# Kernel optimization log

Hardware: AMD Instinct MI355X
Metric: run time of the kernel (lower is better)

The kernel has to match this reference:

```python
import jax, jax.numpy as jnp
import numpy as np
import math

B, L, D, H = 2, 4096, 1024, 16
DH = D // H


def _build_table(seq_len):
    # Faithful port of build_hierarchical_index_lookup_table (static, host-side).
    assert seq_len & (seq_len - 1) == 0
    levels = int(math.log2(seq_len))
    max_valid = 2 * seq_len - 3
    idx = np.full((seq_len, levels), -1, dtype=np.int64)
    cm = np.zeros((seq_len, levels), dtype=bool)
    for n in range(seq_len):
        c = n
        for lvl in range(levels):
            if lvl == 0:
                nxt = c ^ 1
                pair = c
            else:
                nxt = (c // 2 + seq_len) ^ 1
                pair = c // 2 + seq_len
            if nxt > max_valid:
                break
            if pair < nxt:
                cm[n, lvl] = True
            idx[n, lvl] = nxt
            c = nxt
    return idx, cm


def setup_inputs() -> dict:
    rng = jax.random.key(0)
    ks = jax.random.split(rng, 8)
    s = 0.02  # init scale for weights
    idx, cm = _build_table(L)
    return {
        "query": jax.random.normal(ks[0], (B, L, D), jnp.float32),
        "key": jax.random.normal(ks[1], (B, L, D), jnp.float32),
        "value": jax.random.normal(ks[2], (B, L, D), jnp.float32),
        "Wq": jax.random.normal(ks[3], (D, D), jnp.float32) * s,
        "Wk": jax.random.normal(ks[4], (D, D), jnp.float32) * s,
        "Wv": jax.random.normal(ks[5], (D, D), jnp.float32) * s,
        "Wo": jax.random.normal(ks[6], (D, D), jnp.float32) * s,
        "bo": jax.random.normal(ks[7], (D,), jnp.float32) * s,
        "idx_table": jnp.asarray(idx),        # [L, log2(L)] int64
        "causal_mask": jnp.asarray(cm),       # [L, log2(L)] bool
    }


def reference(query, key, value, Wq, Wk, Wv, Wo, bo, idx_table, causal_mask):
    Bq, Lq, Dm = query.shape
    scale = 1.0 / math.sqrt(DH)

    def heads(x, W):  # nn.Linear (no bias) + split heads -> [B,H,L,Dh]
        return (x @ W.T).reshape(Bq, Lq, H, DH).transpose(0, 2, 1, 3)

    Q = heads(query, Wq)
    K = heads(key, Wk)
    V = heads(value, Wv)

    # Build binary-tree hierarchy. Pair weights come from softmax of ZERO
    # logits (Q_parent starts as zeros in the source), so w0 = w1 = 0.5 exactly.
    Ks, Vs = [K], [V]
    while Ks[-1].shape[2] > 1:
        k, v = Ks[-1], Vs[-1]
        Lc = k.shape[2]
        k2 = k.reshape(Bq, H, Lc // 2, 2, DH)
        v2 = v.reshape(Bq, H, Lc // 2, 2, DH)
        Ks.append(0.5 * (k2[:, :, :, 0] + k2[:, :, :, 1]))
        Vs.append(v2[:, :, :, 0] + v2[:, :, :, 1])
    flatK = jnp.concatenate(Ks, axis=2)  # [B,H,2L-1,Dh]
    flatV = jnp.concatenate(Vs, axis=2)

    # Gather neighbor nodes across levels: [B,H,L,levels,Dh]
    nk = flatK[:, :, idx_table]
    nv = flatV[:, :, idx_table]

    self_logits = jnp.einsum('bhnd,bhnd->bhn', Q, K) * scale
    nbr_logits = jnp.einsum('bhld,bhlnd->bhln', Q, nk) * scale
    nbr_logits = jnp.where(causal_mask[None, None], -jnp.inf, nbr_logits)

    all_logits = jnp.concatenate([self_logits[..., None], nbr_logits], axis=-1)
    w = jax.nn.softmax(all_logits, axis=-1)           # [B,H,L,1+levels]
    all_v = jnp.concatenate([V[:, :, :, None, :], nv], axis=3)
    out = jnp.einsum('bhln,bhlnd->bhld', w, all_v)    # [B,H,L,Dh]
    out = out.transpose(0, 2, 1, 3).reshape(Bq, Lq, Dm)
    return out @ Wo.T + bo
```

## Files before the change

### kernel.cpp

```cpp
#include <hip/hip_runtime.h>
#include <cstdint>
#include <cstddef>


typedef __bf16 bf16;
typedef __bf16 bf16x8 __attribute__((ext_vector_type(8)));
typedef __bf16 bf16x4 __attribute__((ext_vector_type(4)));
typedef float  f32x4  __attribute__((ext_vector_type(4)));

#define L_SEQ  4096
#define NFLAT  8192

__device__ __forceinline__ int off_l(int l) { return 8192 - (8192 >> l); }

__device__ __forceinline__ void glds16(const bf16* g, bf16* l) {
  __builtin_amdgcn_global_load_lds(
      (const __attribute__((address_space(1))) unsigned int*)g,
      (__attribute__((address_space(3))) unsigned int*)l, 16, 0, 0);
}

#define MEMFENCE asm volatile("" ::: "memory")
__device__ __forceinline__ void barrier_raw() {
  MEMFENCE; __builtin_amdgcn_s_barrier(); MEMFENCE;
}

__device__ __forceinline__ int swz(int b) { return b ^ (((b >> 9) & 1) << 5); }
__device__ __forceinline__ int la(int row, int col) {
  return ((((row >> 4) << 1) + (col >> 5)) << 10) + ((row & 15) << 6) + ((col & 31) << 1);
}

__global__ __launch_bounds__(256) void cvtall_kernel(
    const float* __restrict__ q, const float* __restrict__ k, const float* __restrict__ v,
    const float* __restrict__ wq, const float* __restrict__ wk,
    const float* __restrict__ wv, const float* __restrict__ wo,
    bf16* __restrict__ qx, bf16* __restrict__ kx, bf16* __restrict__ vx,
    bf16* __restrict__ wqx, bf16* __restrict__ wkx, bf16* __restrict__ wvx,
    bf16* __restrict__ wox) {
  for (int i = blockIdx.x * 256 + threadIdx.x; i < 3670016; i += 524288) {
    int g = i;
    const float* s; bf16* d;
    if (g < 3145728) {
      const int t = g >> 20; g &= 1048575;
      s = (t == 0) ? q : (t == 1) ? k : v;
      d = (t == 0) ? qx : (t == 1) ? kx : vx;
    } else {
      int gg = g - 3145728;
      const int t = gg >> 17; g = gg & 131071;
      s = (t == 0) ? wq : (t == 1) ? wk : (t == 2) ? wv : wo;
      d = (t == 0) ? wqx : (t == 1) ? wkx : (t == 2) ? wvx : wox;
    }
    const float4 v0 = ((const float4*)s)[(size_t)g * 2];
    const float4 v1 = ((const float4*)s)[(size_t)g * 2 + 1];
    bf16x8 o;
    o[0] = (bf16)v0.x; o[1] = (bf16)v0.y; o[2] = (bf16)v0.z; o[3] = (bf16)v0.w;
    o[4] = (bf16)v1.x; o[5] = (bf16)v1.y; o[6] = (bf16)v1.z; o[7] = (bf16)v1.w;
    *(bf16x8*)(d + (size_t)g * 8) = o;
  }
}

#define BUFB 32768

__device__ __forceinline__ void stage_tile(const bf16* __restrict__ A,
                                           const bf16* __restrict__ W,
                                           int tm, int tn, int k0,
                                           char* buf, int tid, int wid) {
  bf16* Ad = (bf16*)buf;
  bf16* Bd = (bf16*)(buf + 16384);
#pragma unroll
  for (int i = 0; i < 4; i++) {
    const int d  = i * 4096 + tid * 16;
    const int lb = swz(d);
    const int row = ((lb >> 10) >> 1) * 16 + ((lb >> 6) & 15);
    const int col = ((lb >> 10) & 1) * 32 + ((lb & 63) >> 1);
    glds16(A + (size_t)(tm * 128 + row) * 1024 + k0 + col, Ad + ((i * 4096 + wid * 1024) >> 1));
    glds16(W + (size_t)(tn * 128 + row) * 1024 + k0 + col, Bd + ((i * 4096 + wid * 1024) >> 1));
  }
}

__device__ __forceinline__ void gemm8_core(const bf16* __restrict__ A,
                                           const bf16* __restrict__ W,
                                           int tm, int tn, char* lds,
                                           f32x4 (&acc)[4][4]) {
  const int tid  = threadIdx.x;
  const int wid  = tid >> 6, lane = tid & 63;
  const int wm   = wid >> 1, wn = wid & 1;
  const int laneR  = lane & 15;
  const int laneC8 = (lane >> 4) * 8;

  stage_tile(A, W, tm, tn, 0, lds, tid, wid);

  for (int u = 0; u < 16; ++u) {
    asm volatile("s_waitcnt vmcnt(0)" ::: "memory");
    barrier_raw();
    if (u + 1 < 16)
      stage_tile(A, W, tm, tn, (u + 1) << 6, lds + ((u + 1) & 1) * BUFB, tid, wid);

    const char* Ab = lds + (u & 1) * BUFB;
    const char* Bb = Ab + 16384;
    bf16x8 af[4][2], bfr[4][2];
#pragma unroll
    for (int f = 0; f < 4; f++)
#pragma unroll
      for (int ks = 0; ks < 2; ks++)
        af[f][ks] = *(const bf16x8*)(Ab + swz(la(wm * 64 + f * 16 + laneR, ks * 32 + laneC8)));
#pragma unroll
    for (int j = 0; j < 4; j++)
#pragma unroll
      for (int ks = 0; ks < 2; ks++)
        bfr[j][ks] = *(const bf16x8*)(Bb + swz(la(wn * 64 + j * 16 + laneR, ks * 32 + laneC8)));

    __builtin_amdgcn_s_setprio(1);
#pragma unroll
    for (int f = 0; f < 4; f++)
#pragma unroll
      for (int j = 0; j < 4; j++)
#pragma unroll
        for (int ks = 0; ks < 2; ks++)
          acc[f][j] = __builtin_amdgcn_mfma_f32_16x16x32_bf16(
              af[f][ks], bfr[j][ks], acc[f][j], 0, 0, 0);
    __builtin_amdgcn_s_setprio(0);
  }
}

__device__ __forceinline__ void tile_map(int bid, int& tm, int& tn) {
  const int xcd = bid & 7, q = bid >> 3;
  tm = xcd * 8 + (q >> 3);
  tn = q & 7;
}

__global__ __launch_bounds__(256, 2) void gemm8_qkv_kernel(
    const bf16* __restrict__ qx, const bf16* __restrict__ kx, const bf16* __restrict__ vx,
    const bf16* __restrict__ wq, const bf16* __restrict__ wk, const bf16* __restrict__ wv,
    bf16* __restrict__ Qb, bf16* __restrict__ fK, bf16* __restrict__ fV) {
  __shared__ __align__(16) char lds[2 * BUFB];
  const int z = blockIdx.y;
  const bf16* A = (z == 0) ? qx : (z == 1) ? kx : vx;
  const bf16* W = (z == 0) ? wq : (z == 1) ? wk : wv;
  bf16* D       = (z == 0) ? Qb : (z == 1) ? fK : fV;
  const int lstr = (z == 0) ? L_SEQ : NFLAT;
  int tm, tn; tile_map(blockIdx.x, tm, tn);
  f32x4 acc[4][4] = {};
  gemm8_core(A, W, tm, tn, lds, acc);

  const int lane = threadIdx.x & 63, wid = threadIdx.x >> 6;
  const int rl0 = (wid >> 1) * 64 + (lane >> 4) * 4;
  const int cl0 = (wid & 1) * 64 + (lane & 15);
#pragma unroll
  for (int i = 0; i < 4; i++)
#pragma unroll
    for (int j = 0; j < 4; j++)
#pragma unroll
      for (int r = 0; r < 4; r++) {
        const int m = tm * 128 + rl0 + i * 16 + r;
        const int n = tn * 128 + cl0 + j * 16;
        const int b = m >> 12, l = m & 4095;
        const int h = n >> 6,  dh = n & 63;
        D[((size_t)(b * 16 + h) * lstr + l) * 64 + dh] = (bf16)acc[i][j][r];
      }

  if (z != 0) {
    bf16* Ct = (bf16*)lds;
    barrier_raw();
#pragma unroll
    for (int i = 0; i < 4; i++)
#pragma unroll
      for (int j = 0; j < 4; j++)
#pragma unroll
        for (int r = 0; r < 4; r++)
          Ct[(rl0 + i * 16 + r) * 132 + (cl0 + j * 16)] = (bf16)acc[i][j][r];
    barrier_raw();

    const int g2 = threadIdx.x >> 7;
    const int c  = threadIdx.x & 127;
    const int h  = tn * 2 + (c >> 6), dh = c & 63;
    const int b  = (tm * 128) >> 12;
    const int lbase = ((tm * 128) & 4095) + g2 * 64;
    const size_t fb = (size_t)(b * 16 + h) * NFLAT * 64 + dh;
    float pk[7];
#pragma unroll
    for (int i = 0; i < 64; i++) {
      float ck = (float)Ct[(g2 * 64 + i) * 132 + c];
#pragma unroll
      for (int l = 1; l <= 6; l++) {
        if (((i + 1) & ((1 << l) - 1)) != 0) { pk[l] = ck; break; }
        ck += pk[l];
        const int j = (lbase + i) >> l;
        D[fb + (size_t)(off_l(l) + j) * 64] =
            (bf16)(z == 1 ? ck * (1.0f / (1 << l)) : ck);
      }
    }
  }
}

__global__ __launch_bounds__(256, 2) void gemm8_out_kernel(
    const bf16* __restrict__ Ob, const bf16* __restrict__ wo,
    const float* __restrict__ bo, float* __restrict__ out) {
  __shared__ __align__(16) char lds[2 * BUFB];
  int tm, tn; tile_map(blockIdx.x, tm, tn);
  f32x4 acc[4][4] = {};
  gemm8_core(Ob, wo, tm, tn, lds, acc);
  const int lane = threadIdx.x & 63, wid = threadIdx.x >> 6;
  const int m0 = tm * 128 + (wid >> 1) * 64 + (lane >> 4) * 4;
  const int n0 = tn * 128 + (wid & 1) * 64 + (lane & 15);
#pragma unroll
  for (int i = 0; i < 4; i++)
#pragma unroll
    for (int j = 0; j < 4; j++)
#pragma unroll
      for (int r = 0; r < 4; r++) {
        const int m = m0 + i * 16 + r;
        const int n = n0 + j * 16;
        out[(size_t)m * 1024 + n] = acc[i][j][r] + bo[n];
      }
}

__global__ __launch_bounds__(64) void tree_l712(bf16* __restrict__ fK, bf16* __restrict__ fV) {
  __shared__ float Ks[64 * 64];
  __shared__ float Vs[64 * 64];
  const int bh = blockIdx.x, d = threadIdx.x;
  const size_t fb = (size_t)bh * NFLAT * 64;
#pragma unroll 8
  for (int i = 0; i < 64; i++) {
    Ks[i * 64 + d] = (float)fK[fb + (size_t)(8064 + i) * 64 + d];
    Vs[i * 64 + d] = (float)fV[fb + (size_t)(8064 + i) * 64 + d];
  }
#pragma unroll
  for (int l = 7; l <= 12; l++) {
    const int cnt = 4096 >> l;
    for (int j = 0; j < cnt; j++) {
      const float k = (Ks[(2 * j) * 64 + d] + Ks[(2 * j + 1) * 64 + d]) * 0.5f;
      const float v =  Vs[(2 * j) * 64 + d] + Vs[(2 * j + 1) * 64 + d];
      Ks[j * 64 + d] = k;
      Vs[j * 64 + d] = v;
      fK[fb + (size_t)(off_l(l) + j) * 64 + d] = (bf16)k;
      fV[fb + (size_t)(off_l(l) + j) * 64 + d] = (bf16)v;
    }
  }
}

__global__ __launch_bounds__(64) void attn_kernel(
    const bf16* __restrict__ Qb, const bf16* __restrict__ fK,
    const bf16* __restrict__ fV, bf16* __restrict__ Ob) {
  __shared__ __align__(16) unsigned short Kl[68 * 64];
  __shared__ __align__(16) unsigned short Vl[68 * 64];
  const int t0  = blockIdx.x * 64;
  const int bh  = blockIdx.y;
  const int tid = threadIdx.x;
  const size_t fb = (size_t)bh * NFLAT * 64;

  for (int u = tid; u < 68 * 8; u += 64) {
    const int r = u >> 3, c = u & 7;
    int flat;
    if      (r < 32) flat = 4096 + (t0 >> 1) + r;
    else if (r < 48) flat = 6144 + (t0 >> 2) + (r - 32);
    else if (r < 56) flat = 7168 + (t0 >> 3) + (r - 48);
    else if (r < 60) flat = 7680 + (t0 >> 4) + (r - 56);
    else if (r < 62) flat = 7936 + (t0 >> 5) + (r - 60);
    else { const int l = r - 56; flat = (8192 - (8192 >> l) + (t0 >> l)) ^ 1; }
    const int cc = c ^ (r & 7);
    const uint4 kk = *(const uint4*)((const char*)(fK + fb + (size_t)flat * 64) + c * 16);
    const uint4 vv = *(const uint4*)((const char*)(fV + fb + (size_t)flat * 64) + c * 16);
    *(uint4*)((char*)Kl + r * 128 + cc * 16) = kk;
    *(uint4*)((char*)Vl + r * 128 + cc * 16) = vv;
  }
  __syncthreads();

  const int n = t0 + tid;
  int rows[13];
#pragma unroll
  for (int l = 1; l < 12; l++) {
    int r;
    if (l <= 5) r = (64 - (128 >> l)) + (((n >> l) ^ 1) - (t0 >> l));
    else        r = 62 + (l - 6);
    rows[l + 1] = r;
  }

  float q[64];
  const bf16* Qr = Qb + ((size_t)bh * L_SEQ + n) * 64;
#pragma unroll
  for (int c = 0; c < 8; c++) {
    bf16x8 v = *(const bf16x8*)(Qr + c * 8);
#pragma unroll
    for (int j = 0; j < 8; j++) q[c * 8 + j] = (float)v[j];
  }

  float lg[13];
  {
    const bf16* Ks0 = fK + fb + (size_t)(t0 + tid) * 64;
    const bf16* Kn0 = fK + fb + (size_t)(t0 + (tid ^ 1)) * 64;
    float a0 = 0.f, a1 = 0.f;
#pragma unroll
    for (int c = 0; c < 8; c++) {
      const bf16x8 s = *(const bf16x8*)(Ks0 + c * 8);
      const bf16x8 t = *(const bf16x8*)(Kn0 + c * 8);
#pragma unroll
      for (int j = 0; j < 8; j++) { a0 += q[c * 8 + j] * (float)s[j]; a1 += q[c * 8 + j] * (float)t[j]; }
    }
    lg[0] = a0 * 0.125f; lg[1] = a1 * 0.125f;
  }
#pragma unroll
  for (int v = 2; v < 13; v++) {
    const int r = rows[v];
    float a = 0.f;
#pragma unroll
    for (int c = 0; c < 8; c++) {
      const int cc = c ^ (r & 7);
      const bf16x8 kv = *(const bf16x8*)((const char*)Kl + r * 128 + cc * 16);
#pragma unroll
      for (int j = 0; j < 8; j++) a += q[c * 8 + j] * (float)kv[j];
    }
    lg[v] = a * 0.125f;
  }
#pragma unroll
  for (int v = 1; v < 13; v++)
    if (!((n >> (v - 1)) & 1)) lg[v] = -1e30f;

  float mx = lg[0];
#pragma unroll
  for (int v = 1; v < 13; v++) mx = fmaxf(mx, lg[v]);
  float w[13], s = 0.f;
#pragma unroll
  for (int v = 0; v < 13; v++) { w[v] = __expf(lg[v] - mx); s += w[v]; }
  const float inv = 1.0f / s;

  float o[64];
#pragma unroll
  for (int d = 0; d < 64; d++) o[d] = 0.f;
  {
    const bf16* Vs0 = fV + fb + (size_t)(t0 + tid) * 64;
    const bf16* Vn0 = fV + fb + (size_t)(t0 + (tid ^ 1)) * 64;
    const float w0 = w[0], w1 = w[1];
#pragma unroll
    for (int c = 0; c < 8; c++) {
      const bf16x8 s0 = *(const bf16x8*)(Vs0 + c * 8);
      const bf16x8 t1 = *(const bf16x8*)(Vn0 + c * 8);
#pragma unroll
      for (int j = 0; j < 8; j++) o[c * 8 + j] += w0 * (float)s0[j] + w1 * (float)t1[j];
    }
  }
#pragma unroll
  for (int v = 2; v < 13; v++) {
    const int r = rows[v];
    const float wv = w[v];
#pragma unroll
    for (int c = 0; c < 8; c++) {
      const int cc = c ^ (r & 7);
      const bf16x8 vv = *(const bf16x8*)((const char*)Vl + r * 128 + cc * 16);
#pragma unroll
      for (int j = 0; j < 8; j++) o[c * 8 + j] += wv * (float)vv[j];
    }
  }

  bf16* Or = Ob + ((size_t)(bh >> 4) * L_SEQ + n) * 1024 + (size_t)(bh & 15) * 64;
#pragma unroll
  for (int c = 0; c < 8; c++) {
    bf16x8 ov;
#pragma unroll
    for (int j = 0; j < 8; j++) ov[j] = (bf16)(o[c * 8 + j] * inv);
    *(bf16x8*)(Or + c * 8) = ov;
  }
}

extern "C" void kernel_launch(void* const* d_in, const int* in_sizes, int n_in,
                              void* d_out, int out_size, void* d_ws, size_t ws_size,
                              hipStream_t stream) {
  const float* query = (const float*)d_in[0];
  const float* key   = (const float*)d_in[1];
  const float* value = (const float*)d_in[2];
  const float* Wq    = (const float*)d_in[3];
  const float* Wk    = (const float*)d_in[4];
  const float* Wv    = (const float*)d_in[5];
  const float* Wo    = (const float*)d_in[6];
  const float* bo    = (const float*)d_in[7];
  float* out = (float*)d_out;

  char* ws = (char*)d_ws;
  size_t off = 0;
  auto take = [&](size_t bytes) -> void* {
    void* p = ws + off;
    off += (bytes + 255) & ~(size_t)255;
    return p;
  };
  const size_t XB = (size_t)8192 * 1024 * 2;
  const size_t WB = (size_t)1024 * 1024 * 2;
  bf16* qx  = (bf16*)take(XB);
  bf16* kx  = (bf16*)take(XB);
  bf16* vx  = (bf16*)take(XB);
  bf16* wqx = (bf16*)take(WB);
  bf16* wkx = (bf16*)take(WB);
  bf16* wvx = (bf16*)take(WB);
  bf16* wox = (bf16*)take(WB);
  bf16* Qb  = (bf16*)take((size_t)32 * L_SEQ * 64 * 2);
  bf16* fK  = (bf16*)take((size_t)32 * NFLAT * 64 * 2);
  bf16* fV  = (bf16*)take((size_t)32 * NFLAT * 64 * 2);
  bf16* Ob  = qx;
  (void)in_sizes; (void)n_in; (void)out_size; (void)ws_size;

  cvtall_kernel<<<2048, 256, 0, stream>>>(
      query, key, value, Wq, Wk, Wv, Wo, qx, kx, vx, wqx, wkx, wvx, wox);

  gemm8_qkv_kernel<<<dim3(512, 3), 256, 0, stream>>>(qx, kx, vx, wqx, wkx, wvx, Qb, fK, fV);

  tree_l712<<<32, 64, 0, stream>>>(fK, fV);

  attn_kernel<<<dim3(64, 32), 64, 0, stream>>>(Qb, fK, fV, Ob);

  gemm8_out_kernel<<<512, 256, 0, stream>>>(Ob, wox, bo, out);
}
```

Before: 159.5 us.

## Fuse fp32-to-bf16 activation conversion into QKV GEMM operand staging

Drops the separate pass that converted the query/key/value activations to bf16. The QKV GEMM now stages fp32 activation tiles straight into LDS and converts them to bf16 in registers before the MFMAs. Only the weights still get a small separate conversion kernel. This removes a full read-write round trip of three 8192x1024 tensors, but doubles the bytes staged per A-tile, halves the K step per barrier (32 iterations instead of 16), and adds conversion work to the inner loop.

```diff
diff --git a/kernel.cpp b/kernel.cpp
--- a/kernel.cpp
+++ b/kernel.cpp
@@ -5,7 +5,6 @@
 
 typedef __bf16 bf16;
 typedef __bf16 bf16x8 __attribute__((ext_vector_type(8)));
-typedef __bf16 bf16x4 __attribute__((ext_vector_type(4)));
 typedef float  f32x4  __attribute__((ext_vector_type(4)));
 
 #define L_SEQ  4096
@@ -13,7 +12,7 @@
 
 __device__ __forceinline__ int off_l(int l) { return 8192 - (8192 >> l); }
 
-__device__ __forceinline__ void glds16(const bf16* g, bf16* l) {
+__device__ __forceinline__ void glds16(const void* g, void* l) {
   __builtin_amdgcn_global_load_lds(
       (const __attribute__((address_space(1))) unsigned int*)g,
       (__attribute__((address_space(3))) unsigned int*)l, 16, 0, 0);
@@ -29,32 +28,171 @@
   return ((((row >> 4) << 1) + (col >> 5)) << 10) + ((row & 15) << 6) + ((col & 31) << 1);
 }
 
-__global__ __launch_bounds__(256) void cvtall_kernel(
-    const float* __restrict__ q, const float* __restrict__ k, const float* __restrict__ v,
+__global__ __launch_bounds__(256) void cvtw_kernel(
     const float* __restrict__ wq, const float* __restrict__ wk,
     const float* __restrict__ wv, const float* __restrict__ wo,
-    bf16* __restrict__ qx, bf16* __restrict__ kx, bf16* __restrict__ vx,
     bf16* __restrict__ wqx, bf16* __restrict__ wkx, bf16* __restrict__ wvx,
     bf16* __restrict__ wox) {
-  for (int i = blockIdx.x * 256 + threadIdx.x; i < 3670016; i += 524288) {
-    int g = i;
-    const float* s; bf16* d;
-    if (g < 3145728) {
-      const int t = g >> 20; g &= 1048575;
-      s = (t == 0) ? q : (t == 1) ? k : v;
-      d = (t == 0) ? qx : (t == 1) ? kx : vx;
-    } else {
-      int gg = g - 3145728;
-      const int t = gg >> 17; g = gg & 131071;
-      s = (t == 0) ? wq : (t == 1) ? wk : (t == 2) ? wv : wo;
-      d = (t == 0) ? wqx : (t == 1) ? wkx : (t == 2) ? wvx : wox;
-    }
+  for (int i = blockIdx.x * 256 + threadIdx.x; i < 524288; i += 65536) {
+    const int t = i >> 17; const int g = i & 131071;
+    const float* s = (t == 0) ? wq : (t == 1) ? wk : (t == 2) ? wv : wo;
+    bf16*        d = (t == 0) ? wqx : (t == 1) ? wkx : (t == 2) ? wvx : wox;
     const float4 v0 = ((const float4*)s)[(size_t)g * 2];
     const float4 v1 = ((const float4*)s)[(size_t)g * 2 + 1];
     bf16x8 o;
     o[0] = (bf16)v0.x; o[1] = (bf16)v0.y; o[2] = (bf16)v0.z; o[3] = (bf16)v0.w;
     o[4] = (bf16)v1.x; o[5] = (bf16)v1.y; o[6] = (bf16)v1.z; o[7] = (bf16)v1.w;
     *(bf16x8*)(d + (size_t)g * 8) = o;
+  }
+}
+
+__device__ __forceinline__ void stage_A32(const float* __restrict__ A,
+                                          int tm, int k0, char* buf,
+                                          int tid, int wid) {
+#pragma unroll
+  for (int i = 0; i < 4; i++) {
+    const int d  = i * 4096 + tid * 16;
+    const int lb = swz(d);
+    const int row = ((lb >> 10) >> 1) * 16 + ((lb >> 6) & 15);
+    const int col = ((lb >> 10) & 1) * 16 + ((lb & 63) >> 2);
+    glds16(A + (size_t)(tm * 128 + row) * 1024 + k0 + col,
+           buf + i * 4096 + wid * 1024);
+  }
+}
+__device__ __forceinline__ void stage_B64(const bf16* __restrict__ W,
+                                          int tn, int k0, char* buf,
+                                          int tid, int wid) {
+#pragma unroll
+  for (int i = 0; i < 4; i++) {
+    const int d  = i * 4096 + tid * 16;
+    const int lb = swz(d);
+    const int row = ((lb >> 10) >> 1) * 16 + ((lb >> 6) & 15);
+    const int col = ((lb >> 10) & 1) * 32 + ((lb & 63) >> 1);
+    glds16(W + (size_t)(tn * 128 + row) * 1024 + k0 + col,
+           buf + i * 4096 + wid * 1024);
+  }
+}
+
+__device__ __forceinline__ void gemmf_core(const float* __restrict__ A,
+                                           const bf16* __restrict__ W,
+                                           int tm, int tn, char* lds,
+                                           f32x4 (&acc)[4][4]) {
+  const int tid  = threadIdx.x;
+  const int wid  = tid >> 6, lane = tid & 63;
+  const int wm   = wid >> 1, wn = wid & 1;
+  const int laneR  = lane & 15;
+  const int k16    = lane >> 4;
+  char* Al = lds;
+  char* Bl = lds + 32768;
+
+  stage_A32(A, tm, 0, Al, tid, wid);
+  stage_B64(W, tn, 0, Bl, tid, wid);
+
+  for (int s = 0; s < 32; ++s) {
+    asm volatile("s_waitcnt vmcnt(0)" ::: "memory");
+    barrier_raw();
+    if (s + 1 < 32) stage_A32(A, tm, (s + 1) << 5, Al + ((s + 1) & 1) * 16384, tid, wid);
+    if (!(s & 1) && (s >> 1) + 1 < 16)
+      stage_B64(W, tn, ((s >> 1) + 1) << 6, Bl + (((s >> 1) + 1) & 1) * 16384, tid, wid);
+
+    const char* Ab = Al + (s & 1) * 16384;
+    const char* Bb = Bl + ((s >> 1) & 1) * 16384;
+    const int kc = (s & 1) * 32;
+
+    bf16x8 af[4], bfr[4];
+#pragma unroll
+    for (int f = 0; f < 4; f++) {
+      const int row = wm * 64 + f * 16 + laneR;
+      const f32x4 a0 = *(const f32x4*)(Ab + swz(la(row, k16 * 16)));
+      const f32x4 a1 = *(const f32x4*)(Ab + swz(la(row, k16 * 16 + 8)));
+      bf16x8 o;
+      o[0] = (bf16)a0[0]; o[1] = (bf16)a0[1]; o[2] = (bf16)a0[2]; o[3] = (bf16)a0[3];
+      o[4] = (bf16)a1[0]; o[5] = (bf16)a1[1]; o[6] = (bf16)a1[2]; o[7] = (bf16)a1[3];
+      af[f] = o;
+    }
+#pragma unroll
+    for (int j = 0; j < 4; j++) {
+      const int row = wn * 64 + j * 16 + laneR;
+      bfr[j] = *(const bf16x8*)(Bb + swz(la(row, kc + k16 * 8)));
+    }
+
+    __builtin_amdgcn_s_setprio(1);
+#pragma unroll
+    for (int f = 0; f < 4; f++)
+#pragma unroll
+      for (int j = 0; j < 4; j++)
+        acc[f][j] = __builtin_amdgcn_mfma_f32_16x16x32_bf16(af[f], bfr[j], acc[f][j], 0, 0, 0);
+    __builtin_amdgcn_s_setprio(0);
+  }
+}
+
+__device__ __forceinline__ void tile_map(int bid, int& tm, int& tn) {
+  const int xcd = bid & 7, q = bid >> 3;
+  tm = xcd * 8 + (q >> 3);
+  tn = q & 7;
+}
+
+__global__ __launch_bounds__(256, 2) void gemmf_qkv_kernel(
+    const float* __restrict__ qf, const float* __restrict__ kf, const float* __restrict__ vf,
+    const bf16* __restrict__ wq, const bf16* __restrict__ wk, const bf16* __restrict__ wv,
+    bf16* __restrict__ Qb, bf16* __restrict__ fK, bf16* __restrict__ fV) {
+  __shared__ __align__(16) char lds[65536];
+  const int z = blockIdx.y;
+  const float* A = (z == 0) ? qf : (z == 1) ? kf : vf;
+  const bf16*  W = (z == 0) ? wq : (z == 1) ? wk : wv;
+  bf16* D        = (z == 0) ? Qb : (z == 1) ? fK : fV;
+  const int lstr = (z == 0) ? L_SEQ : NFLAT;
+  int tm, tn; tile_map(blockIdx.x, tm, tn);
+  f32x4 acc[4][4] = {};
+  gemmf_core(A, W, tm, tn, lds, acc);
+
+  const int lane = threadIdx.x & 63, wid = threadIdx.x >> 6;
+  const int rl0 = (wid >> 1) * 64 + (lane >> 4) * 4;
+  const int cl0 = (wid & 1) * 64 + (lane & 15);
+#pragma unroll
+  for (int i = 0; i < 4; i++)
+#pragma unroll
+    for (int j = 0; j < 4; j++)
+#pragma unroll
+      for (int r = 0; r < 4; r++) {
+        const int m = tm * 128 + rl0 + i * 16 + r;
+        const int n = tn * 128 + cl0 + j * 16;
+        const int b = m >> 12, l = m & 4095;
+        const int h = n >> 6,  dh = n & 63;
+        D[((size_t)(b * 16 + h) * lstr + l) * 64 + dh] = (bf16)acc[i][j][r];
+      }
+
+  if (z != 0) {
+    bf16* Ct = (bf16*)lds;
+    barrier_raw();
+#pragma unroll
+    for (int i = 0; i < 4; i++)
+#pragma unroll
+      for (int j = 0; j < 4; j++)
+#pragma unroll
+        for (int r = 0; r < 4; r++)
+          Ct[(rl0 + i * 16 + r) * 132 + (cl0 + j * 16)] = (bf16)acc[i][j][r];
+    barrier_raw();
+
+    const int g2 = threadIdx.x >> 7;
+    const int c  = threadIdx.x & 127;
+    const int h  = tn * 2 + (c >> 6), dh = c & 63;
+    const int b  = (tm * 128) >> 12;
+    const int lbase = ((tm * 128) & 4095) + g2 * 64;
+    const size_t fb = (size_t)(b * 16 + h) * NFLAT * 64 + dh;
+    float pk[7];
+#pragma unroll
+    for (int i = 0; i < 64; i++) {
+      float ck = (float)Ct[(g2 * 64 + i) * 132 + c];
+#pragma unroll
+      for (int l = 1; l <= 6; l++) {
+        if (((i + 1) & ((1 << l) - 1)) != 0) { pk[l] = ck; break; }
+        ck += pk[l];
+        const int j = (lbase + i) >> l;
+        D[fb + (size_t)(off_l(l) + j) * 64] =
+            (bf16)(z == 1 ? ck * (1.0f / (1 << l)) : ck);
+      }
+    }
   }
 }
 
@@ -119,76 +257,6 @@
           acc[f][j] = __builtin_amdgcn_mfma_f32_16x16x32_bf16(
               af[f][ks], bfr[j][ks], acc[f][j], 0, 0, 0);
     __builtin_amdgcn_s_setprio(0);
-  }
-}
-
-__device__ __forceinline__ void tile_map(int bid, int& tm, int& tn) {
-  const int xcd = bid & 7, q = bid >> 3;
-  tm = xcd * 8 + (q >> 3);
-  tn = q & 7;
-}
-
-__global__ __launch_bounds__(256, 2) void gemm8_qkv_kernel(
-    const bf16* __restrict__ qx, const bf16* __restrict__ kx, const bf16* __restrict__ vx,
-    const bf16* __restrict__ wq, const bf16* __restrict__ wk, const bf16* __restrict__ wv,
-    bf16* __restrict__ Qb, bf16* __restrict__ fK, bf16* __restrict__ fV) {
-  __shared__ __align__(16) char lds[2 * BUFB];
-  const int z = blockIdx.y;
-  const bf16* A = (z == 0) ? qx : (z == 1) ? kx : vx;
-  const bf16* W = (z == 0) ? wq : (z == 1) ? wk : wv;
-  bf16* D       = (z == 0) ? Qb : (z == 1) ? fK : fV;
-  const int lstr = (z == 0) ? L_SEQ : NFLAT;
-  int tm, tn; tile_map(blockIdx.x, tm, tn);
-  f32x4 acc[4][4] = {};
-  gemm8_core(A, W, tm, tn, lds, acc);
-
-  const int lane = threadIdx.x & 63, wid = threadIdx.x >> 6;
-  const int rl0 = (wid >> 1) * 64 + (lane >> 4) * 4;
-  const int cl0 = (wid & 1) * 64 + (lane & 15);
-#pragma unroll
-  for (int i = 0; i < 4; i++)
-#pragma unroll
-    for (int j = 0; j < 4; j++)
-#pragma unroll
-      for (int r = 0; r < 4; r++) {
-        const int m = tm * 128 + rl0 + i * 16 + r;
-        const int n = tn * 128 + cl0 + j * 16;
-        const int b = m >> 12, l = m & 4095;
-        const int h = n >> 6,  dh = n & 63;
-        D[((size_t)(b * 16 + h) * lstr + l) * 64 + dh] = (bf16)acc[i][j][r];
-      }
-
-  if (z != 0) {
-    bf16* Ct = (bf16*)lds;
-    barrier_raw();
-#pragma unroll
-    for (int i = 0; i < 4; i++)
-#pragma unroll
-      for (int j = 0; j < 4; j++)
-#pragma unroll
-        for (int r = 0; r < 4; r++)
-          Ct[(rl0 + i * 16 + r) * 132 + (cl0 + j * 16)] = (bf16)acc[i][j][r];
-    barrier_raw();
-
-    const int g2 = threadIdx.x >> 7;
-    const int c  = threadIdx.x & 127;
-    const int h  = tn * 2 + (c >> 6), dh = c & 63;
-    const int b  = (tm * 128) >> 12;
-    const int lbase = ((tm * 128) & 4095) + g2 * 64;
-    const size_t fb = (size_t)(b * 16 + h) * NFLAT * 64 + dh;
-    float pk[7];
-#pragma unroll
-    for (int i = 0; i < 64; i++) {
-      float ck = (float)Ct[(g2 * 64 + i) * 132 + c];
-#pragma unroll
-      for (int l = 1; l <= 6; l++) {
-        if (((i + 1) & ((1 << l) - 1)) != 0) { pk[l] = ck; break; }
-        ck += pk[l];
-        const int j = (lbase + i) >> l;
-        D[fb + (size_t)(off_l(l) + j) * 64] =
-            (bf16)(z == 1 ? ck * (1.0f / (1 << l)) : ck);
-      }
-    }
   }
 }
 
@@ -381,11 +449,7 @@
     off += (bytes + 255) & ~(size_t)255;
     return p;
   };
-  const size_t XB = (size_t)8192 * 1024 * 2;
   const size_t WB = (size_t)1024 * 1024 * 2;
-  bf16* qx  = (bf16*)take(XB);
-  bf16* kx  = (bf16*)take(XB);
-  bf16* vx  = (bf16*)take(XB);
   bf16* wqx = (bf16*)take(WB);
   bf16* wkx = (bf16*)take(WB);
   bf16* wvx = (bf16*)take(WB);
@@ -393,13 +457,13 @@
   bf16* Qb  = (bf16*)take((size_t)32 * L_SEQ * 64 * 2);
   bf16* fK  = (bf16*)take((size_t)32 * NFLAT * 64 * 2);
   bf16* fV  = (bf16*)take((size_t)32 * NFLAT * 64 * 2);
-  bf16* Ob  = qx;
+  bf16* Ob  = (bf16*)take((size_t)8192 * 1024 * 2);
   (void)in_sizes; (void)n_in; (void)out_size; (void)ws_size;
 
-  cvtall_kernel<<<2048, 256, 0, stream>>>(
-      query, key, value, Wq, Wk, Wv, Wo, qx, kx, vx, wqx, wkx, wvx, wox);
-
-  gemm8_qkv_kernel<<<dim3(512, 3), 256, 0, stream>>>(qx, kx, vx, wqx, wkx, wvx, Qb, fK, fV);
+  cvtw_kernel<<<256, 256, 0, stream>>>(Wq, Wk, Wv, Wo, wqx, wkx, wvx, wox);
+
+  gemmf_qkv_kernel<<<dim3(512, 3), 256, 0, stream>>>(
+      query, key, value, wqx, wkx, wvx, Qb, fK, fV);
 
   tree_l712<<<32, 64, 0, stream>>>(fK, fV);
 
```

Result: faster. 155.9 us (median of 5 runs) (-2.3%).
